# Kernel optimization log

Measured on AMD Instinct MI355X. Metric: run time of the kernel, lower is better.

The kernel has to match this reference:

```python
import jax, jax.numpy as jnp
import numpy as np

N, E, G = 20000, 320000, 256
CAT, CONT, NEL = 16, 8, 9
HC, HE, HID, H, OUT = 32, 32, 64, 4, 128


def _gatv2(h, src, tgt, ee, Wl, bl, Wr, br, We, att, bias):
    # PyG GATv2Conv (eval mode, flow=source_to_target): messages aggregated at tgt
    n = h.shape[0]
    Hh, C = att.shape
    xl = (h @ Wl + bl).reshape(n, Hh, C)   # source transform
    xr = (h @ Wr + br).reshape(n, Hh, C)   # target transform
    ep = (ee @ We).reshape(-1, Hh, C)      # edge transform (no bias in PyG)
    m = jax.nn.leaky_relu(xl[src] + xr[tgt] + ep, 0.2)  # [E,H,C]
    e = jnp.einsum('ehc,hc->eh', m, att)                # [E,H]
    emax = jax.ops.segment_max(e, tgt, num_segments=n)
    p = jnp.exp(e - emax[tgt])
    denom = jax.ops.segment_sum(p, tgt, num_segments=n)
    alpha = p / (denom[tgt] + 1e-16)
    out = jax.ops.segment_sum(alpha[..., None] * xl[src], tgt, num_segments=n)
    return out.reshape(n, Hh * C) + bias


def setup_inputs() -> dict:
    key = jax.random.key(0)
    k = jax.random.split(key, 26)
    f = jnp.float32
    def w(kk, i, o):
        return jax.random.normal(kk, (i, o), f) / np.float32(np.sqrt(i))
    return {
        'x': jax.random.normal(k[0], (N, CAT + CONT), f),
        'edge_index': jax.random.randint(k[1], (2, E), 0, N, jnp.int32),
        'edge_attr': jax.random.uniform(k[2], (E, NEL), f),
        'batch': jnp.sort(jax.random.randint(k[3], (N,), 0, G, jnp.int32)),
        'W_cat': w(k[4], CAT, HC), 'b_cat': jnp.zeros((HC,), f),
        'W_e': w(k[5], NEL, HE), 'b_e': jnp.zeros((HE,), f),
        'W_init': w(k[6], CONT + HC, HID), 'b_init': jnp.zeros((HID,), f),
        'Wl1': w(k[7], HID, H * HID), 'bl1': jnp.zeros((H * HID,), f),
        'Wr1': w(k[8], HID, H * HID), 'br1': jnp.zeros((H * HID,), f),
        'We1': w(k[9], HE, H * HID),
        'att1': jax.random.normal(k[10], (H, HID), f) / np.float32(np.sqrt(HID)),
        'bias1': jnp.zeros((H * HID,), f),
        'Wl2': w(k[11], H * HID, HID), 'bl2': jnp.zeros((HID,), f),
        'Wr2': w(k[12], H * HID, HID), 'br2': jnp.zeros((HID,), f),
        'We2': w(k[13], HE, HID),
        'att2': jax.random.normal(k[14], (1, HID), f) / np.float32(np.sqrt(HID)),
        'bias2': jnp.zeros((HID,), f),
        'W_out': w(k[15], HID, OUT), 'b_out': jnp.zeros((OUT,), f),
    }


def reference(x, edge_index, edge_attr, batch,
              W_cat, b_cat, W_e, b_e, W_init, b_init,
              Wl1, bl1, Wr1, br1, We1, att1, bias1,
              Wl2, bl2, Wr2, br2, We2, att2, bias2,
              W_out, b_out):
    n = x.shape[0]
    f = x.dtype
    s = jax.nn.relu(x[:, :CAT] @ W_cat + b_cat)
    h = jnp.concatenate([x[:, CAT:], s], axis=1)
    h = jax.nn.relu(h @ W_init + b_init)
    ee = edge_attr @ W_e + b_e                       # [E, HE]
    src, tgt = edge_index[0], edge_index[1]
    # PyG GATv2Conv add_self_loops=True, fill_value='mean' on edge features
    cnt = jax.ops.segment_sum(jnp.ones((src.shape[0],), f), tgt, num_segments=n)
    loop_attr = jax.ops.segment_sum(ee, tgt, num_segments=n) / jnp.maximum(cnt, 1.0)[:, None]
    ar = jnp.arange(n, dtype=src.dtype)
    src2 = jnp.concatenate([src, ar])
    tgt2 = jnp.concatenate([tgt, ar])
    ee2 = jnp.concatenate([ee, loop_attr], axis=0)
    h = jax.nn.elu(_gatv2(h, src2, tgt2, ee2, Wl1, bl1, Wr1, br1, We1, att1, bias1))
    h = jax.nn.elu(_gatv2(h, src2, tgt2, ee2, Wl2, bl2, Wr2, br2, We2, att2, bias2))
    # global_mean_pool over graphs
    gcnt = jax.ops.segment_sum(jnp.ones((n,), f), batch, num_segments=G)
    pooled = jax.ops.segment_sum(h, batch, num_segments=G) / jnp.maximum(gcnt, 1.0)[:, None]
    return pooled @ W_out + b_out
```

## Files before the change

### kernel.cpp

```cpp
#include <hip/hip_runtime.h>
#include <hip/hip_bf16.h>

#define NN 20000
#define EE 320000
#define GG 256

__device__ __forceinline__ float lanebc(float v, int l){
  return __uint_as_float(__builtin_amdgcn_readlane(__float_as_uint(v), (unsigned)l));
}
__device__ __forceinline__ int lanebci(int v, int l){
  return __builtin_amdgcn_readlane(v, (unsigned)l);
}
__device__ __forceinline__ float wave_sum(float v){
  #pragma unroll
  for(int m=32;m>0;m>>=1) v += __shfl_xor(v, m, 64);
  return v;
}
__device__ __forceinline__ float elu(float o){
  return (o > 0.f) ? o : (__expf(o) - 1.f);
}
__device__ __forceinline__ float pexp(float e){ return __expf(fminf(e, 60.f)); }
__device__ __forceinline__ float bf2f(ushort u){ return __uint_as_float((unsigned)u << 16); }
__device__ __forceinline__ ushort f2bf(float f){
  unsigned x = __float_as_uint(f);
  return (ushort)((x + 0x7FFFu + ((x >> 16) & 1u)) >> 16);
}
__device__ __forceinline__ float2 up2(unsigned w){
  return make_float2(__uint_as_float(w << 16), __uint_as_float(w & 0xFFFF0000u));
}

__global__ void k_weights(const float* __restrict__ We9, const float* __restrict__ be,
                          const float* __restrict__ We1, const float* __restrict__ We2,
                          const float* __restrict__ Wl1, const float* __restrict__ Wl2,
                          const float* __restrict__ Wr2,
                          float* __restrict__ Wf1, float* __restrict__ bf1,
                          float* __restrict__ Wf2, float* __restrict__ bf2,
                          float4* __restrict__ Wl1p4, float4* __restrict__ Wl2p4,
                          float4* __restrict__ Wr2p4){
  const int b = blockIdx.x;
  const int tid = threadIdx.x;
  if (b < 48){
    const int idx = (b%16)*256 + tid;
    const int seg = b/16;
    if (seg == 0){
      const int k4 = idx>>8, c = idx&255;
      Wl1p4[idx] = make_float4(Wl1[(4*k4+0)*256+c], Wl1[(4*k4+1)*256+c],
                               Wl1[(4*k4+2)*256+c], Wl1[(4*k4+3)*256+c]);
    } else if (seg == 1){
      const int k4 = idx>>6, cc = idx&63;
      Wl2p4[idx] = make_float4(Wl2[(4*k4+0)*64+cc], Wl2[(4*k4+1)*64+cc],
                               Wl2[(4*k4+2)*64+cc], Wl2[(4*k4+3)*64+cc]);
    } else {
      const int k4 = idx>>6, cc = idx&63;
      Wr2p4[idx] = make_float4(Wr2[(4*k4+0)*64+cc], Wr2[(4*k4+1)*64+cc],
                               Wr2[(4*k4+2)*64+cc], Wr2[(4*k4+3)*64+cc]);
    }
  } else if (b == 48){
    const int c = tid;
    #pragma unroll
    for (int j=0;j<9;j++){
      float a = 0.f;
      #pragma unroll
      for (int k=0;k<32;k++) a += We9[j*32+k]*We1[k*256+c];
      Wf1[j*256+c] = a;
    }
    float bb = 0.f;
    #pragma unroll
    for (int k=0;k<32;k++) bb += be[k]*We1[k*256+c];
    bf1[c] = bb;
  } else {
    if (tid < 64){
      const int c = tid;
      #pragma unroll
      for (int j=0;j<9;j++){
        float a = 0.f;
        #pragma unroll
        for (int k=0;k<32;k++) a += We9[j*32+k]*We2[k*64+c];
        Wf2[j*64+c] = a;
      }
      float bb = 0.f;
      #pragma unroll
      for (int k=0;k<32;k++) bb += be[k]*We2[k*64+c];
      bf2[c] = bb;
    }
  }
}

__global__ void k_edge_acc(const int* __restrict__ ei, const float* __restrict__ ea,
                           float* __restrict__ loopA, int* __restrict__ cnt){
  const int g = blockIdx.x*16 + (threadIdx.x>>4);
  const int j = threadIdx.x & 15;
  if (g >= EE) return;
  const int t = ei[EE + g];
  if (j < 9)       atomicAdd(&loopA[t*12 + j], ea[(size_t)g*9 + j]);
  else if (j == 9) atomicAdd(&cnt[t], 1);
}

__global__ void k_alloc(const int* __restrict__ cnt, int* __restrict__ start, int* __restrict__ counter){
  int i = blockIdx.x*blockDim.x + threadIdx.x;
  if (i < NN) start[i] = atomicAdd(counter, cnt[i]);
}

__global__ void k_scatter(const int* __restrict__ ei, const int* __restrict__ start,
                          int* __restrict__ fill, int* __restrict__ csr,
                          int* __restrict__ srcp, int* __restrict__ tgtp){
  int e = blockIdx.x*blockDim.x + threadIdx.x;
  if (e >= EE) return;
  int t = ei[EE + e];
  int p = start[t] + atomicAdd(&fill[t], 1);
  csr[p] = e;
  srcp[p] = ei[e];
  tgtp[p] = t;
}

__global__ __launch_bounds__(256) void k_xlxr1f(
    const float* __restrict__ x, const float* __restrict__ Wcat,
    const float* __restrict__ bcat, const float* __restrict__ Wini,
    const float* __restrict__ bini, const float* __restrict__ Wl,
    const float* __restrict__ bl, const float* __restrict__ Wr,
    const float* __restrict__ br, ushort* __restrict__ h0b,
    ushort* __restrict__ xl, ushort* __restrict__ xr)
{
  const int n0 = blockIdx.x*8;
  const int tid = threadIdx.x;
  __shared__ float xs[8][25];
  __shared__ float sv[8][33];
  __shared__ __align__(16) float hsT[64][8];
  if (tid < 192){ int n=tid/24, j=tid%24; xs[n][j] = x[(size_t)(n0+n)*24 + j]; }
  __syncthreads();
  {
    const int n = tid>>5, cc = tid&31;
    float a = bcat[cc];
    #pragma unroll
    for (int k=0;k<16;k++) a += xs[n][k]*Wcat[k*32+cc];
    sv[n][cc] = fmaxf(a, 0.f);
  }
  __syncthreads();
  #pragma unroll
  for (int i=tid;i<512;i+=256){
    const int n = i>>6, c = i&63;
    float a = bini[c];
    #pragma unroll
    for (int k=0;k<8;k++)  a += xs[n][16+k]*Wini[k*64+c];
    #pragma unroll
    for (int k=0;k<32;k++) a += sv[n][k]*Wini[(8+k)*64+c];
    const float r = fmaxf(a, 0.f);
    hsT[c][n] = r;
    h0b[(size_t)(n0+n)*64 + c] = f2bf(r);
  }
  __syncthreads();
  const int c = tid;
  float accl[8], accr[8];
  const float blv = bl[c], brv = br[c];
  #pragma unroll
  for(int n=0;n<8;n++){ accl[n]=blv; accr[n]=brv; }
  for(int k=0;k<64;k++){
    const float wl = Wl[k*256 + c];
    const float wr = Wr[k*256 + c];
    const float4 ha = *(const float4*)&hsT[k][0];
    const float4 hb = *(const float4*)&hsT[k][4];
    accl[0]+=ha.x*wl; accr[0]+=ha.x*wr; accl[1]+=ha.y*wl; accr[1]+=ha.y*wr;
    accl[2]+=ha.z*wl; accr[2]+=ha.z*wr; accl[3]+=ha.w*wl; accr[3]+=ha.w*wr;
    accl[4]+=hb.x*wl; accr[4]+=hb.x*wr; accl[5]+=hb.y*wl; accr[5]+=hb.y*wr;
    accl[6]+=hb.z*wl; accr[6]+=hb.z*wr; accl[7]+=hb.w*wl; accr[7]+=hb.w*wr;
  }
  #pragma unroll
  for(int n=0;n<8;n++){
    xl[(size_t)(n0+n)*256 + c] = f2bf(accl[n]);
    xr[(size_t)(n0+n)*256 + c] = f2bf(accr[n]);
  }
}

template<int F>
__global__ __launch_bounds__(256) void k_score(const float* __restrict__ ea, const int* __restrict__ csr,
                        const int* __restrict__ srcp, const int* __restrict__ tgtp,
                        const ushort* __restrict__ xl, const ushort* __restrict__ xr,
                        const float* __restrict__ Wf, const float* __restrict__ bf,
                        const float* __restrict__ att, float* __restrict__ esc)
{
  constexpr int HP  = (F == 256) ? 2 : 1;
  constexpr int CPL = (F == 256) ? 8 : 4;
  const int tid  = threadIdx.x;
  const int lane = tid & 63;
  const int w    = tid >> 6;
  const int p0   = blockIdx.x * 64;

  __shared__ float ea_sT[9][64];
  __shared__ float Wf_s[9*F];
  __shared__ float bf_s[F];
  __shared__ int csr_s[64], src_s[64], tgt_s[64];

  if (tid < 64) { csr_s[tid] = csr[p0+tid]; src_s[tid] = srcp[p0+tid]; tgt_s[tid] = tgtp[p0+tid]; }
  __syncthreads();
  for (int i = tid; i < 576; i += 256){ int j = i>>6, ed = i&63; ea_sT[j][ed] = ea[(size_t)csr_s[ed]*9 + j]; }
  for (int i = tid; i < (9*F)/4; i += 256) ((float4*)Wf_s)[i] = ((const float4*)Wf)[i];
  if (tid < F) bf_s[tid] = bf[tid];
  __syncthreads();

  const int g = lane >> 4, t = lane & 15;
  const int eb = w*16 + g*4;

  #pragma unroll
  for (int hp = 0; hp < HP; ++hp) {
    const int c = hp*(F/HP) + t*CPL;
    float bfv[CPL];
    *(float4*)&bfv[0] = *(const float4*)&bf_s[c];
    if (CPL==8) *(float4*)&bfv[4] = *(const float4*)&bf_s[c+4];
    float acc[4][CPL];
    #pragma unroll
    for (int j=0;j<4;j++)
      #pragma unroll
      for(int q=0;q<CPL;q++) acc[j][q]=bfv[q];
    #pragma unroll
    for (int k=0;k<9;k++){
      const float4 ev = *(const float4*)&ea_sT[k][eb];
      float wv[CPL];
      *(float4*)&wv[0] = *(const float4*)&Wf_s[k*F + c];
      if (CPL==8) *(float4*)&wv[4] = *(const float4*)&Wf_s[k*F + c + 4];
      #pragma unroll
      for (int q=0;q<CPL;q++){
        acc[0][q] += ev.x*wv[q]; acc[1][q] += ev.y*wv[q];
        acc[2][q] += ev.z*wv[q]; acc[3][q] += ev.w*wv[q];
      }
    }
    float attv[CPL];
    *(float4*)&attv[0] = *(const float4*)&att[c];
    if (CPL==8) *(float4*)&attv[4] = *(const float4*)&att[c+4];
    float partial[4];
    #pragma unroll
    for (int j=0;j<4;j++){
      const int s  = src_s[eb+j];
      const int tg = tgt_s[eb+j];
      float xlv[CPL], xrv[CPL];
      if (CPL==8){
        const uint4 a = *(const uint4*)&xl[(size_t)s*F + c];
        const uint4 b = *(const uint4*)&xr[(size_t)tg*F + c];
        float2 p;
        p=up2(a.x); xlv[0]=p.x; xlv[1]=p.y;  p=up2(a.y); xlv[2]=p.x; xlv[3]=p.y;
        p=up2(a.z); xlv[4]=p.x; xlv[5]=p.y;  p=up2(a.w); xlv[6]=p.x; xlv[7]=p.y;
        p=up2(b.x); xrv[0]=p.x; xrv[1]=p.y;  p=up2(b.y); xrv[2]=p.x; xrv[3]=p.y;
        p=up2(b.z); xrv[4]=p.x; xrv[5]=p.y;  p=up2(b.w); xrv[6]=p.x; xrv[7]=p.y;
      } else {
        const uint2 a = *(const uint2*)&xl[(size_t)s*F + c];
        const uint2 b = *(const uint2*)&xr[(size_t)tg*F + c];
        float2 p;
        p=up2(a.x); xlv[0]=p.x; xlv[1]=p.y;  p=up2(a.y); xlv[2]=p.x; xlv[3]=p.y;
        p=up2(b.x); xrv[0]=p.x; xrv[1]=p.y;  p=up2(b.y); xrv[2]=p.x; xrv[3]=p.y;
      }
      float sum = 0.f;
      #pragma unroll
      for (int q=0;q<CPL;q++){
        float m = acc[j][q] + xlv[q] + xrv[q];
        m = (m >= 0.f) ? m : 0.2f*m;
        sum += attv[q]*m;
      }
      partial[j] = sum;
    }
    #pragma unroll
    for (int j=0;j<4;j++){
      partial[j] += __shfl_xor(partial[j], 1, 64);
      partial[j] += __shfl_xor(partial[j], 2, 64);
      partial[j] += __shfl_xor(partial[j], 4, 64);
      if (F==64) partial[j] += __shfl_xor(partial[j], 8, 64);
    }
    if (F==256){
      if ((t & 7) == 0){
        const int h = hp*2 + (t>>3);
        #pragma unroll
        for (int j=0;j<4;j++) esc[(size_t)h*EE + p0 + eb + j] = partial[j];
      }
    } else {
      if (t == 0){
        #pragma unroll
        for (int j=0;j<4;j++) esc[p0 + eb + j] = partial[j];
      }
    }
  }
}

__global__ __launch_bounds__(256) void k_agg1(
    const float* __restrict__ loopA, const int* __restrict__ cnt,
    const int* __restrict__ start, const int* __restrict__ srcp,
    const ushort* __restrict__ h0b, const ushort* __restrict__ xl, const ushort* __restrict__ xr,
    const float* __restrict__ Wf, const float* __restrict__ bf,
    const float* __restrict__ att, const float* __restrict__ esc,
    float* __restrict__ zb)
{
  const int t = blockIdx.x*4 + (threadIdx.x>>6);
  const int c = threadIdx.x & 63;
  const int st = start[t], dg = cnt[t];

  float epb[4];
  if (dg > 0){
    const float invc = 1.f/(float)dg;
    float la[9];
    #pragma unroll
    for (int j=0;j<9;j++) la[j] = loopA[t*12+j]*invc;
    #pragma unroll
    for (int hd=0;hd<4;hd++){
      float ep = bf[hd*64+c];
      #pragma unroll
      for (int j=0;j<9;j++) ep += la[j]*Wf[j*256 + hd*64 + c];
      epb[hd] = ep;
    }
  } else {
    #pragma unroll
    for (int hd=0;hd<4;hd++) epb[hd]=0.f;
  }
  const float h0t = bf2f(h0b[(size_t)t*64 + c]);
  float preg[4], den[4], z[4];
  #pragma unroll
  for (int hd=0;hd<4;hd++){
    float m = bf2f(xl[(size_t)t*256 + hd*64 + c]) + bf2f(xr[(size_t)t*256 + hd*64 + c]) + epb[hd];
    m = (m>=0.f)? m : 0.2f*m;
    const float pS = pexp(wave_sum(att[hd*64+c]*m));
    den[hd] = pS;
    z[hd] = pS*h0t;
  }

  int sL = 0;
  #pragma unroll
  for (int hd=0;hd<4;hd++) preg[hd] = 0.f;
  if (c < dg){
    sL = srcp[st+c];
    #pragma unroll
    for (int hd=0;hd<4;hd++) preg[hd] = pexp(esc[(size_t)hd*EE + st + c]);
  }
  #pragma unroll
  for (int hd=0;hd<4;hd++) den[hd] += wave_sum(preg[hd]);

  const int d1 = min(dg,64);
  for (int i=0;i<d1;i+=4){
    const int s0=lanebci(sL,i), s1=lanebci(sL,i+1), s2=lanebci(sL,i+2), s3=lanebci(sL,i+3);
    const float v0=bf2f(h0b[(size_t)s0*64+c]), v1=bf2f(h0b[(size_t)s1*64+c]);
    const float v2=bf2f(h0b[(size_t)s2*64+c]), v3=bf2f(h0b[(size_t)s3*64+c]);
    #pragma unroll
    for (int hd=0;hd<4;hd++){
      z[hd] += lanebc(preg[hd],i)*v0;
      z[hd] += lanebc(preg[hd],i+1)*v1;
      z[hd] += lanebc(preg[hd],i+2)*v2;
      z[hd] += lanebc(preg[hd],i+3)*v3;
    }
  }
  for (int i=64;i<dg;i++){
    const float hv = bf2f(h0b[(size_t)srcp[st+i]*64+c]);
    #pragma unroll
    for (int hd=0;hd<4;hd++){
      const float pp = pexp(esc[(size_t)hd*EE + st + i]);
      den[hd] += pp;
      z[hd] += pp*hv;
    }
  }
  #pragma unroll
  for (int hd=0;hd<4;hd++) zb[(size_t)t*256 + hd*64 + c] = z[hd]/(den[hd]+1e-16f);
}

__global__ __launch_bounds__(256) void k_h1xlxr2(
    const float* __restrict__ zb, const float4* __restrict__ Wl1p4,
    const float* __restrict__ bl1, const float* __restrict__ bias1,
    const float4* __restrict__ Wl2p4, const float* __restrict__ bl2,
    const float4* __restrict__ Wr2p4, const float* __restrict__ br2,
    ushort* __restrict__ xl2, ushort* __restrict__ xr2)
{
  const int n0 = blockIdx.x*16;
  const int tid = threadIdx.x;
  __shared__ float zT[256*20];
  __shared__ __align__(16) float4 hs[64][17];
  #pragma unroll
  for (int j=0;j<16;j++) zT[tid*20 + j] = zb[(size_t)(n0+j)*256 + tid];
  __syncthreads();
  {
    const int c = tid, hd = c>>6;
    float acc[16];
    const float b = bl1[c] + bias1[c];
    #pragma unroll
    for (int n=0;n<16;n++) acc[n]=b;
    #pragma unroll 4
    for (int k4=0;k4<16;k4++){
      const float4 w4 = Wl1p4[k4*256 + c];
      #pragma unroll
      for (int kk=0;kk<4;kk++){
        const float wk = (kk==0)?w4.x:(kk==1)?w4.y:(kk==2)?w4.z:w4.w;
        const float* zr = &zT[(hd*64 + k4*4 + kk)*20];
        const float4 z0 = *(const float4*)&zr[0];
        const float4 z1 = *(const float4*)&zr[4];
        const float4 z2 = *(const float4*)&zr[8];
        const float4 z3 = *(const float4*)&zr[12];
        acc[0]+=z0.x*wk; acc[1]+=z0.y*wk; acc[2]+=z0.z*wk; acc[3]+=z0.w*wk;
        acc[4]+=z1.x*wk; acc[5]+=z1.y*wk; acc[6]+=z1.z*wk; acc[7]+=z1.w*wk;
        acc[8]+=z2.x*wk; acc[9]+=z2.y*wk; acc[10]+=z2.z*wk; acc[11]+=z2.w*wk;
        acc[12]+=z3.x*wk; acc[13]+=z3.y*wk; acc[14]+=z3.z*wk; acc[15]+=z3.w*wk;
      }
    }
    float* hsf = (float*)hs;
    const int base = (c>>2)*17*4 + (c&3);
    #pragma unroll
    for (int n=0;n<16;n++) hsf[base + n*4] = elu(acc[n]);
  }
  __syncthreads();
  {
    const int cc = tid & 63, ng = tid >> 6;
    float al[4], ar[4];
    const float bl = bl2[cc], br = br2[cc];
    #pragma unroll
    for (int j=0;j<4;j++){ al[j]=bl; ar[j]=br; }
    #pragma unroll 4
    for (int k4=0;k4<64;k4++){
      const float4 wl = Wl2p4[k4*64 + cc];
      const float4 wr = Wr2p4[k4*64 + cc];
      #pragma unroll
      for (int j=0;j<4;j++){
        const float4 hv = hs[k4][ng*4 + j];
        al[j] += hv.x*wl.x + hv.y*wl.y + hv.z*wl.z + hv.w*wl.w;
        ar[j] += hv.x*wr.x + hv.y*wr.y + hv.z*wr.z + hv.w*wr.w;
      }
    }
    #pragma unroll
    for (int j=0;j<4;j++){
      xl2[(size_t)(n0+ng*4+j)*64 + cc] = f2bf(al[j]);
      xr2[(size_t)(n0+ng*4+j)*64 + cc] = f2bf(ar[j]);
    }
  }
}

__global__ __launch_bounds__(256) void k_agg2(
    const float* __restrict__ loopA, const int* __restrict__ cnt,
    const int* __restrict__ start, const int* __restrict__ srcp,
    const ushort* __restrict__ xl, const ushort* __restrict__ xr,
    const float* __restrict__ Wf, const float* __restrict__ bf,
    const float* __restrict__ att, const float* __restrict__ bias,
    const float* __restrict__ esc, const int* __restrict__ batch,
    float* __restrict__ pooled, int* __restrict__ gcnt)
{
  const int t = blockIdx.x*4 + (threadIdx.x>>6);
  const int c = threadIdx.x & 63;
  const int st = start[t], dg = cnt[t];

  float ep = 0.f;
  if (dg>0){
    const float invc = 1.f/(float)dg;
    ep = bf[c];
    #pragma unroll
    for (int j=0;j<9;j++) ep += (loopA[t*12+j]*invc)*Wf[j*64+c];
  }
  const float xlt = bf2f(xl[(size_t)t*64+c]);
  float m = xlt + bf2f(xr[(size_t)t*64+c]) + ep;
  m = (m>=0.f)? m : 0.2f*m;
  const float pS = pexp(wave_sum(att[c]*m));

  int sL=0; float preg=0.f;
  if (c<dg){ sL=srcp[st+c]; preg=pexp(esc[st+c]); }
  float den = wave_sum(preg)+pS;
  float z = pS*xlt;
  const int d1=min(dg,64);
  for (int i=0;i<d1;i+=4){
    const int s0=lanebci(sL,i),s1=lanebci(sL,i+1),s2=lanebci(sL,i+2),s3=lanebci(sL,i+3);
    const float p0=lanebc(preg,i),p1=lanebc(preg,i+1),p2=lanebc(preg,i+2),p3=lanebc(preg,i+3);
    const float v0=bf2f(xl[(size_t)s0*64+c]),v1=bf2f(xl[(size_t)s1*64+c]);
    const float v2=bf2f(xl[(size_t)s2*64+c]),v3=bf2f(xl[(size_t)s3*64+c]);
    z += p0*v0; z += p1*v1; z += p2*v2; z += p3*v3;
  }
  for (int i=64;i<dg;i++){
    const float pp=pexp(esc[st+i]); den+=pp;
    z += pp*bf2f(xl[(size_t)srcp[st+i]*64+c]);
  }
  const float o = z/(den+1e-16f)+bias[c];
  const float r = elu(o);
  const int g = batch[t];
  atomicAdd(&pooled[g*64 + c], r);
  if (c == 0) atomicAdd(&gcnt[g], 1);
}

__global__ void k_out(const float* __restrict__ pooled, const int* __restrict__ gcnt,
                      const float* __restrict__ Wout, const float* __restrict__ bout,
                      float* __restrict__ out){
  int g = blockIdx.x, o = threadIdx.x;
  float a = 0.f;
  for(int k=0;k<64;k++) a += pooled[g*64 + k] * Wout[k*128 + o];
  float inv = 1.f / fmaxf((float)gcnt[g], 1.f);
  out[g*128 + o] = a*inv + bout[o];
}

extern "C" void kernel_launch(void* const* d_in, const int* in_sizes, int n_in,
                              void* d_out, int out_size, void* d_ws, size_t ws_size,
                              hipStream_t stream) {
  const float* x    = (const float*)d_in[0];
  const int*   ei   = (const int*)  d_in[1];
  const float* ea   = (const float*)d_in[2];
  const int*   batch= (const int*)  d_in[3];
  const float* Wcat = (const float*)d_in[4];
  const float* bcat = (const float*)d_in[5];
  const float* We   = (const float*)d_in[6];
  const float* be   = (const float*)d_in[7];
  const float* Wini = (const float*)d_in[8];
  const float* bini = (const float*)d_in[9];
  const float* Wl1  = (const float*)d_in[10];
  const float* bl1  = (const float*)d_in[11];
  const float* Wr1  = (const float*)d_in[12];
  const float* br1  = (const float*)d_in[13];
  const float* We1  = (const float*)d_in[14];
  const float* att1 = (const float*)d_in[15];
  const float* bias1= (const float*)d_in[16];
  const float* Wl2  = (const float*)d_in[17];
  const float* bl2  = (const float*)d_in[18];
  const float* Wr2  = (const float*)d_in[19];
  const float* br2  = (const float*)d_in[20];
  const float* We2  = (const float*)d_in[21];
  const float* att2 = (const float*)d_in[22];
  const float* bias2= (const float*)d_in[23];
  const float* Wout = (const float*)d_in[24];
  const float* bout = (const float*)d_in[25];
  float* out = (float*)d_out;
  char* ws = (char*)d_ws;

  size_t off = 0;
  auto alloc = [&](size_t bytes)->char*{ char* p = ws + off; off += (bytes + 255) & ~(size_t)255; return p; };
  ushort* h0b   = (ushort*)alloc((size_t)NN*64*2);
  ushort* xl1   = (ushort*)alloc((size_t)NN*256*2);
  ushort* xr1   = (ushort*)alloc((size_t)NN*256*2);
  float*  zb    = (float*) alloc((size_t)NN*256*4);
  ushort* xl2   = (ushort*)alloc((size_t)NN*64*2);
  ushort* xr2   = (ushort*)alloc((size_t)NN*64*2);
  float*  esc   = (float*) alloc((size_t)EE*4*4);
  float*  esc2  = (float*) alloc((size_t)EE*4);
  float*  Wf1   = (float*) alloc((size_t)9*256*4);
  float*  bf1   = (float*) alloc((size_t)256*4);
  float*  Wf2   = (float*) alloc((size_t)9*64*4);
  float*  bf2   = (float*) alloc((size_t)64*4);
  float4* Wl1p4 = (float4*)alloc((size_t)4096*16);
  float4* Wl2p4 = (float4*)alloc((size_t)4096*16);
  float4* Wr2p4 = (float4*)alloc((size_t)4096*16);
  int*    start = (int*)   alloc((size_t)NN*4);
  int*    csr   = (int*)   alloc((size_t)EE*4);
  int*    srcp  = (int*)   alloc((size_t)EE*4);
  int*    tgtp  = (int*)   alloc((size_t)EE*4);
  const size_t zoff = off;
  float*  loopA = (float*) alloc((size_t)NN*12*4);
  int*    cnt   = (int*)   alloc((size_t)NN*4);
  int*    fill  = (int*)   alloc((size_t)NN*4);
  int*    counter = (int*) alloc(256);
  float*  pooled  = (float*)alloc((size_t)GG*64*4);
  int*    gcnt    = (int*)  alloc((size_t)GG*4);
  const size_t zlen = off - zoff;

  hipMemsetAsync(ws + zoff, 0, zlen, stream);

  k_weights  <<<50, 256, 0, stream>>>(We, be, We1, We2, Wl1, Wl2, Wr2,
                                      Wf1, bf1, Wf2, bf2, Wl1p4, Wl2p4, Wr2p4);
  k_edge_acc <<<EE/16, 256, 0, stream>>>(ei, ea, loopA, cnt);
  k_alloc    <<<(NN+255)/256, 256, 0, stream>>>(cnt, start, counter);
  k_scatter  <<<(EE+255)/256, 256, 0, stream>>>(ei, start, fill, csr, srcp, tgtp);
  k_xlxr1f   <<<NN/8, 256, 0, stream>>>(x, Wcat, bcat, Wini, bini,
                                        Wl1, bl1, Wr1, br1, h0b, xl1, xr1);
  k_score<256><<<EE/64, 256, 0, stream>>>(ea, csr, srcp, tgtp, xl1, xr1, Wf1, bf1, att1, esc);
  k_agg1     <<<NN/4, 256, 0, stream>>>(loopA, cnt, start, srcp, h0b, xl1, xr1, Wf1, bf1, att1, esc, zb);
  k_h1xlxr2  <<<NN/16, 256, 0, stream>>>(zb, Wl1p4, bl1, bias1, Wl2p4, bl2, Wr2p4, br2, xl2, xr2);
  k_score<64><<<EE/64, 256, 0, stream>>>(ea, csr, srcp, tgtp, xl2, xr2, Wf2, bf2, att2, esc2);
  k_agg2     <<<NN/4, 256, 0, stream>>>(loopA, cnt, start, srcp, xl2, xr2, Wf2, bf2, att2, bias2,
                                        esc2, batch, pooled, gcnt);
  k_out      <<<GG, 128, 0, stream>>>(pooled, gcnt, Wout, bout, out);
}
```

Before: 307.1 us.

## Precompute exp in edge-score kernel, store zb in bf16, unroll gathers by 8

The edge-score kernel now stores exp of the clamped scores, so the aggregation kernels read probabilities directly instead of recomputing exp for every edge and head. The intermediate zb buffer between layer-1 aggregation and the next projection is stored as bf16 instead of fp32, halving its write and read traffic. The neighbour gather loops in both aggregation kernels are unrolled from 4 to 8 to keep more loads in flight. The risks are extra rounding from bf16 zb and higher register pressure from the wider unroll.

```diff
diff --git a/kernel.cpp b/kernel.cpp
--- a/kernel.cpp
+++ b/kernel.cpp
@@ -267,12 +267,12 @@
       if ((t & 7) == 0){
         const int h = hp*2 + (t>>3);
         #pragma unroll
-        for (int j=0;j<4;j++) esc[(size_t)h*EE + p0 + eb + j] = partial[j];
+        for (int j=0;j<4;j++) esc[(size_t)h*EE + p0 + eb + j] = pexp(partial[j]);
       }
     } else {
       if (t == 0){
         #pragma unroll
-        for (int j=0;j<4;j++) esc[p0 + eb + j] = partial[j];
+        for (int j=0;j<4;j++) esc[p0 + eb + j] = pexp(partial[j]);
       }
     }
   }
@@ -284,7 +284,7 @@
     const ushort* __restrict__ h0b, const ushort* __restrict__ xl, const ushort* __restrict__ xr,
     const float* __restrict__ Wf, const float* __restrict__ bf,
     const float* __restrict__ att, const float* __restrict__ esc,
-    float* __restrict__ zb)
+    ushort* __restrict__ zb)
 {
   const int t = blockIdx.x*4 + (threadIdx.x>>6);
   const int c = threadIdx.x & 63;
@@ -324,39 +324,40 @@
   if (c < dg){
     sL = srcp[st+c];
     #pragma unroll
-    for (int hd=0;hd<4;hd++) preg[hd] = pexp(esc[(size_t)hd*EE + st + c]);
+    for (int hd=0;hd<4;hd++) preg[hd] = esc[(size_t)hd*EE + st + c];
   }
   #pragma unroll
   for (int hd=0;hd<4;hd++) den[hd] += wave_sum(preg[hd]);
 
   const int d1 = min(dg,64);
-  for (int i=0;i<d1;i+=4){
-    const int s0=lanebci(sL,i), s1=lanebci(sL,i+1), s2=lanebci(sL,i+2), s3=lanebci(sL,i+3);
-    const float v0=bf2f(h0b[(size_t)s0*64+c]), v1=bf2f(h0b[(size_t)s1*64+c]);
-    const float v2=bf2f(h0b[(size_t)s2*64+c]), v3=bf2f(h0b[(size_t)s3*64+c]);
+  for (int i=0;i<d1;i+=8){
+    int ss[8];
+    #pragma unroll
+    for (int u=0;u<8;u++) ss[u] = lanebci(sL, i+u);
+    float vv[8];
+    #pragma unroll
+    for (int u=0;u<8;u++) vv[u] = bf2f(h0b[(size_t)ss[u]*64 + c]);
     #pragma unroll
     for (int hd=0;hd<4;hd++){
-      z[hd] += lanebc(preg[hd],i)*v0;
-      z[hd] += lanebc(preg[hd],i+1)*v1;
-      z[hd] += lanebc(preg[hd],i+2)*v2;
-      z[hd] += lanebc(preg[hd],i+3)*v3;
+      #pragma unroll
+      for (int u=0;u<8;u++) z[hd] += lanebc(preg[hd], i+u)*vv[u];
     }
   }
   for (int i=64;i<dg;i++){
     const float hv = bf2f(h0b[(size_t)srcp[st+i]*64+c]);
     #pragma unroll
     for (int hd=0;hd<4;hd++){
-      const float pp = pexp(esc[(size_t)hd*EE + st + i]);
+      const float pp = esc[(size_t)hd*EE + st + i];
       den[hd] += pp;
       z[hd] += pp*hv;
     }
   }
   #pragma unroll
-  for (int hd=0;hd<4;hd++) zb[(size_t)t*256 + hd*64 + c] = z[hd]/(den[hd]+1e-16f);
+  for (int hd=0;hd<4;hd++) zb[(size_t)t*256 + hd*64 + c] = f2bf(z[hd]/(den[hd]+1e-16f));
 }
 
 __global__ __launch_bounds__(256) void k_h1xlxr2(
-    const float* __restrict__ zb, const float4* __restrict__ Wl1p4,
+    const ushort* __restrict__ zb, const float4* __restrict__ Wl1p4,
     const float* __restrict__ bl1, const float* __restrict__ bias1,
     const float4* __restrict__ Wl2p4, const float* __restrict__ bl2,
     const float4* __restrict__ Wr2p4, const float* __restrict__ br2,
@@ -367,7 +368,7 @@
   __shared__ float zT[256*20];
   __shared__ __align__(16) float4 hs[64][17];
   #pragma unroll
-  for (int j=0;j<16;j++) zT[tid*20 + j] = zb[(size_t)(n0+j)*256 + tid];
+  for (int j=0;j<16;j++) zT[tid*20 + j] = bf2f(zb[(size_t)(n0+j)*256 + tid]);
   __syncthreads();
   {
     const int c = tid, hd = c>>6;
@@ -449,19 +450,22 @@
   const float pS = pexp(wave_sum(att[c]*m));
 
   int sL=0; float preg=0.f;
-  if (c<dg){ sL=srcp[st+c]; preg=pexp(esc[st+c]); }
+  if (c<dg){ sL=srcp[st+c]; preg=esc[st+c]; }
   float den = wave_sum(preg)+pS;
   float z = pS*xlt;
   const int d1=min(dg,64);
-  for (int i=0;i<d1;i+=4){
-    const int s0=lanebci(sL,i),s1=lanebci(sL,i+1),s2=lanebci(sL,i+2),s3=lanebci(sL,i+3);
-    const float p0=lanebc(preg,i),p1=lanebc(preg,i+1),p2=lanebc(preg,i+2),p3=lanebc(preg,i+3);
-    const float v0=bf2f(xl[(size_t)s0*64+c]),v1=bf2f(xl[(size_t)s1*64+c]);
-    const float v2=bf2f(xl[(size_t)s2*64+c]),v3=bf2f(xl[(size_t)s3*64+c]);
-    z += p0*v0; z += p1*v1; z += p2*v2; z += p3*v3;
+  for (int i=0;i<d1;i+=8){
+    int ss[8];
+    #pragma unroll
+    for (int u=0;u<8;u++) ss[u] = lanebci(sL, i+u);
+    float vv[8];
+    #pragma unroll
+    for (int u=0;u<8;u++) vv[u] = bf2f(xl[(size_t)ss[u]*64 + c]);
+    #pragma unroll
+    for (int u=0;u<8;u++) z += lanebc(preg, i+u)*vv[u];
   }
   for (int i=64;i<dg;i++){
-    const float pp=pexp(esc[st+i]); den+=pp;
+    const float pp=esc[st+i]; den+=pp;
     z += pp*bf2f(xl[(size_t)srcp[st+i]*64+c]);
   }
   const float o = z/(den+1e-16f)+bias[c];
@@ -518,7 +522,7 @@
   ushort* h0b   = (ushort*)alloc((size_t)NN*64*2);
   ushort* xl1   = (ushort*)alloc((size_t)NN*256*2);
   ushort* xr1   = (ushort*)alloc((size_t)NN*256*2);
-  float*  zb    = (float*) alloc((size_t)NN*256*4);
+  ushort* zb    = (ushort*)alloc((size_t)NN*256*2);
   ushort* xl2   = (ushort*)alloc((size_t)NN*64*2);
   ushort* xr2   = (ushort*)alloc((size_t)NN*64*2);
   float*  esc   = (float*) alloc((size_t)EE*4*4);
```

After: 437.7 us. +42.5%, slower.
